# Performance work log

Measured on AMD Instinct MI355X. Metric: run time of the kernel, lower is better.

## Reference

```python
import jax, jax.numpy as jnp
import numpy as np

B, L, H, NH, NB = 16, 256, 64, 2, 2
HS = H // NH
MAXLEN, TIME_SPAN, ITEMNUM = 256, 256, 50000
NEG = -4294967295.0  # -2**32 + 1
EPS = 1e-8


def layernorm(x, g, b):
    m = jnp.mean(x, axis=-1, keepdims=True)
    v = jnp.mean((x - m) ** 2, axis=-1, keepdims=True)
    return g * (x - m) / jnp.sqrt(v + EPS) + b


def setup_inputs() -> dict:
    key = jax.random.key(0)
    ks = jax.random.split(key, 24)
    s = 0.02
    inp = {
        "seqs_data": jax.random.randint(ks[0], (B, L), 0, ITEMNUM, dtype=jnp.int32),
        "seqs": jax.random.normal(ks[1], (B, L, H), dtype=jnp.float32),
        "positions": jax.random.randint(ks[2], (B, L), 0, MAXLEN, dtype=jnp.int32),
        "time_matrices": jax.random.randint(ks[3], (B, L, L), 0, TIME_SPAN + 1, dtype=jnp.int32),
        "abs_pos_K_tab": jax.random.normal(ks[4], (MAXLEN, H)) * s,
        "abs_pos_V_tab": jax.random.normal(ks[5], (MAXLEN, H)) * s,
        "time_K_tab": jax.random.normal(ks[6], (TIME_SPAN + 1, H)) * s,
        "time_V_tab": jax.random.normal(ks[7], (TIME_SPAN + 1, H)) * s,
        "Qw": jax.random.normal(ks[8], (NB, H, H)) * s,
        "Qb": jnp.zeros((NB, H)),
        "Kw": jax.random.normal(ks[9], (NB, H, H)) * s,
        "Kb": jnp.zeros((NB, H)),
        "Vw": jax.random.normal(ks[10], (NB, H, H)) * s,
        "Vb": jnp.zeros((NB, H)),
        "ln1_g": jnp.ones((NB, H)), "ln1_b": jnp.zeros((NB, H)),
        "ln2_g": jnp.ones((NB, H)), "ln2_b": jnp.zeros((NB, H)),
        "ffn_W1": jax.random.normal(ks[11], (NB, H, H)) * s,
        "ffn_b1": jnp.zeros((NB, H)),
        "ffn_W2": jax.random.normal(ks[12], (NB, H, H)) * s,
        "ffn_b2": jnp.zeros((NB, H)),
        "last_g": jnp.ones((H,)), "last_b": jnp.zeros((H,)),
    }
    return inp


def _forward(seqs_data, seqs, positions, time_matrices,
             abs_pos_K_tab, abs_pos_V_tab, time_K_tab, time_V_tab,
             Qw, Qb, Kw, Kb, Vw, Vb, ln1_g, ln1_b, ln2_g, ln2_b,
             ffn_W1, ffn_b1, ffn_W2, ffn_b2, last_g, last_b):
    # abs-pos embeddings with padding_idx=0 (zero row, no grad flow to it)
    pos_keep = (positions != 0)[..., None].astype(seqs.dtype)
    abs_pos_K = abs_pos_K_tab[positions] * pos_keep            # [B,L,H]
    abs_pos_V = abs_pos_V_tab[positions] * pos_keep
    time_K = time_K_tab[time_matrices]                         # [B,L,L,H]
    time_V = time_V_tab[time_matrices]
    tmK = time_K.reshape(B, L, L, NH, HS)
    tmV = time_V.reshape(B, L, L, NH, HS)
    aK = abs_pos_K.reshape(B, L, NH, HS)
    aV = abs_pos_V.reshape(B, L, NH, HS)

    timeline_mask = (seqs_data == ITEMNUM - 1)                 # [B,L] True = pad
    keep = (~timeline_mask)[..., None].astype(seqs.dtype)
    seqs = seqs * keep
    causal = ~jnp.tril(jnp.ones((L, L), dtype=bool))           # [L,L] upper tri
    full_mask = timeline_mask[:, None, :, None] | causal[None, None]  # [B,1,L,L]

    for i in range(NB):
        q_in = layernorm(seqs, ln1_g[i], ln1_b[i])
        Q = (q_in @ Qw[i].T + Qb[i]).reshape(B, L, NH, HS)
        K = (seqs @ Kw[i].T + Kb[i]).reshape(B, L, NH, HS)
        V = (seqs @ Vw[i].T + Vb[i]).reshape(B, L, NH, HS)
        aw = (jnp.einsum('blhd,bmhd->bhlm', Q, K)
              + jnp.einsum('blhd,bmhd->bhlm', Q, aK)
              + jnp.einsum('blmhd,blhd->bhlm', tmK, Q)) / (HS ** 0.5)
        aw = jnp.where(full_mask, NEG, aw)
        A = jax.nn.softmax(aw, axis=-1)                        # [B,NH,L,L]
        out = (jnp.einsum('bhlm,bmhd->blhd', A, V)
               + jnp.einsum('bhlm,bmhd->blhd', A, aV)
               + jnp.einsum('bhlm,blmhd->blhd', A, tmV)).reshape(B, L, H)
        seqs = q_in + out
        seqs = layernorm(seqs, ln2_g[i], ln2_b[i])
        h = jax.nn.relu(seqs @ ffn_W1[i].T + ffn_b1[i])
        seqs = (h @ ffn_W2[i].T + ffn_b2[i]) + seqs
        seqs = seqs * keep
    return layernorm(seqs, last_g, last_b)


def reference(seqs_data, seqs, positions, time_matrices,
              abs_pos_K_tab, abs_pos_V_tab, time_K_tab, time_V_tab,
              Qw, Qb, Kw, Kb, Vw, Vb, ln1_g, ln1_b, ln2_g, ln2_b,
              ffn_W1, ffn_b1, ffn_W2, ffn_b2, last_g, last_b):
    return _forward(seqs_data, seqs, positions, time_matrices,
                    abs_pos_K_tab, abs_pos_V_tab, time_K_tab, time_V_tab,
                    Qw, Qb, Kw, Kb, Vw, Vb, ln1_g, ln1_b, ln2_g, ln2_b,
                    ffn_W1, ffn_b1, ffn_W2, ffn_b2, last_g, last_b)
```

## Files before the change

### kernel.cpp

```cpp
#include <hip/hip_runtime.h>
#include <math.h>

#define BATCH 16
#define SEQL  256
#define HDIM  64
#define NBLK  2
#define PADID 49999
#define NEGV  -4294967295.0f
#define LNEPS 1e-8f
#define INV_SQRT_HS 0.17677669529663687f
#define TKC   257
#define TKTLD 260
#define QG    4

__device__ __forceinline__ float waveReduceSum(float v) {
#pragma unroll
    for (int o = 32; o > 0; o >>= 1) v += __shfl_xor(v, o);
    return v;
}

__global__ __launch_bounds__(256) void setup_kernel(
    const float* __restrict__ Qw, const float* __restrict__ Kw,
    const float* __restrict__ Vw, const float* __restrict__ W1,
    const float* __restrict__ W2, const float* __restrict__ tKtab,
    float* __restrict__ QwT, float* __restrict__ KwT, float* __restrict__ VwT,
    float* __restrict__ W1T, float* __restrict__ W2T, float* __restrict__ tKtabT)
{
    __shared__ float tile[64][65];
    const int tid = threadIdx.x;
    const int blk = blockIdx.x;
    if (blk < 10) {
        const float* srcs[10] = {Qw, Qw+4096, Kw, Kw+4096, Vw, Vw+4096,
                                 W1, W1+4096, W2, W2+4096};
        float*       dsts[10] = {QwT, QwT+4096, KwT, KwT+4096, VwT, VwT+4096,
                                 W1T, W1T+4096, W2T, W2T+4096};
        const float* s = srcs[blk];
        float*       d = dsts[blk];
        for (int p = 0; p < 16; ++p) {
            int r = p*4 + (tid>>6), c = tid&63;
            tile[r][c] = s[r*64 + c];
        }
        __syncthreads();
        for (int p = 0; p < 16; ++p) {
            int mth = p*4 + (tid>>6), t = tid&63;
            d[mth*64 + t] = tile[t][mth];
        }
    } else {
        const int s0 = (blk - 10) * 64;
        const int nrows = min(64, TKC - s0);
        for (int p = 0; p < 16; ++p) {
            int rr = p*4 + (tid>>6), c = tid&63;
            if (rr < nrows) tile[rr][c] = tKtab[(size_t)(s0+rr)*64 + c];
        }
        __syncthreads();
        for (int p = 0; p < 16; ++p) {
            int dd = p*4 + (tid>>6), cc = tid&63;
            if (cc < nrows) tKtabT[dd*TKTLD + s0 + cc] = tile[cc][dd];
        }
    }
}

__global__ __launch_bounds__(256) void prep_kernel(
    const float* __restrict__ xin, const int* __restrict__ seqs_data,
    const int* __restrict__ positions,
    const float* __restrict__ QwT, const float* __restrict__ Qb,
    const float* __restrict__ KwT, const float* __restrict__ Kb,
    const float* __restrict__ VwT, const float* __restrict__ Vb,
    const float* __restrict__ g1, const float* __restrict__ b1,
    const float* __restrict__ apK, const float* __restrict__ apV,
    float* __restrict__ q_in, float* __restrict__ Qo,
    float* __restrict__ KpT, float* __restrict__ Vp)
{
    const int w = threadIdx.x >> 6;
    const int t = threadIdx.x & 63;
    const int row0 = blockIdx.x * 4;
    const int row = row0 + w;
    float x = xin[(size_t)row * HDIM + t];
    if (seqs_data[row] == PADID) x = 0.f;

    float mean = waveReduceSum(x) * (1.f / HDIM);
    float d = x - mean;
    float var = waveReduceSum(d * d) * (1.f / HDIM);
    float q = g1[t] * d / sqrtf(var + LNEPS) + b1[t];

    __shared__ float xs[4][HDIM];
    __shared__ float qs[4][HDIM];
    __shared__ float kx[HDIM][5];
    xs[w][t] = x; qs[w][t] = q;
    q_in[(size_t)row * HDIM + t] = q;

    int pos = positions[row];
    float aK = pos ? apK[(size_t)pos * HDIM + t] : 0.f;
    float aV = pos ? apV[(size_t)pos * HDIM + t] : 0.f;

    float aq = 0.f, ak = 0.f, av = 0.f;
#pragma unroll 16
    for (int mth = 0; mth < 64; ++mth) {
        float qm = qs[w][mth], xm = xs[w][mth];
        aq += qm * QwT[mth*64 + t];
        ak += xm * KwT[mth*64 + t];
        av += xm * VwT[mth*64 + t];
    }
    Qo[(size_t)row * HDIM + t] = aq + Qb[t];
    Vp[(size_t)row * HDIM + t] = av + Vb[t] + aV;
    kx[t][w] = ak + Kb[t] + aK;
    __syncthreads();
    const int f = threadIdx.x >> 2, j = threadIdx.x & 3;
    KpT[(size_t)f * 4096 + row0 + j] = kx[f][j];
}

__global__ __launch_bounds__(256) void attn_kernel(
    const float* __restrict__ Qo, const float* __restrict__ KpT,
    const float* __restrict__ Vp, const float* __restrict__ q_in,
    const int* __restrict__ seqs_data, const int* __restrict__ tmat,
    const float* __restrict__ tVtab, const float* __restrict__ tKtabT,
    float* __restrict__ x2)
{
    const int hw  = blockIdx.x;
    const int blk = (hw & 7) * 128 + (hw >> 3);
    const int b   = blk >> 6;
    const int l0  = (blk & 63) << 2;
    const int row0 = b * SEQL + l0;
    const int tid = threadIdx.x;
    const int m = tid;
    const int lane = tid & 63, wv = tid >> 6;

    __shared__ float qs_l[QG][HDIM];
    __shared__ float Tk_l[QG][2][TKTLD];
    __shared__ float A_s[QG][2][SEQL];
    __shared__ float Wl[QG][2][TKTLD];
    __shared__ float outred[4][QG][HDIM];
    __shared__ float redm[QG][2][4];
    __shared__ float reds[QG][2][4];

    for (int k = tid; k < QG*2*TKTLD; k += 256) ((float*)Wl)[k] = 0.f;
    qs_l[tid >> 6][tid & 63] = Qo[(size_t)(row0 + (tid >> 6)) * HDIM + (tid & 63)];
    __syncthreads();

    for (int c = tid; c < TKC; c += 256) {
        float a00 = 0.f, a10 = 0.f, a20 = 0.f, a30 = 0.f;
        float a01 = 0.f, a11 = 0.f, a21 = 0.f, a31 = 0.f;
#pragma unroll 8
        for (int dd = 0; dd < 32; ++dd) {
            float tt = tKtabT[dd*TKTLD + c];
            a00 += tt * qs_l[0][dd]; a10 += tt * qs_l[1][dd];
            a20 += tt * qs_l[2][dd]; a30 += tt * qs_l[3][dd];
        }
#pragma unroll 8
        for (int dd = 32; dd < 64; ++dd) {
            float tt = tKtabT[dd*TKTLD + c];
            a01 += tt * qs_l[0][dd]; a11 += tt * qs_l[1][dd];
            a21 += tt * qs_l[2][dd]; a31 += tt * qs_l[3][dd];
        }
        Tk_l[0][0][c] = a00; Tk_l[1][0][c] = a10; Tk_l[2][0][c] = a20; Tk_l[3][0][c] = a30;
        Tk_l[0][1][c] = a01; Tk_l[1][1][c] = a11; Tk_l[2][1][c] = a21; Tk_l[3][1][c] = a31;
    }

    bool qpad[QG]; bool anypad = false;
#pragma unroll
    for (int li = 0; li < QG; ++li) {
        qpad[li] = (seqs_data[row0 + li] == PADID);
        anypad |= qpad[li];
    }
    const int lmax = l0 + QG - 1;

    float kp[64];
    if ((m <= lmax) || anypad) {
#pragma unroll
        for (int dd = 0; dd < 64; ++dd)
            kp[dd] = KpT[(size_t)dd * 4096 + b * SEQL + m];
    } else {
#pragma unroll
        for (int dd = 0; dd < 64; ++dd) kp[dd] = 0.f;
    }
    int tmc[QG];
#pragma unroll
    for (int li = 0; li < QG; ++li)
        tmc[li] = tmat[(size_t)(row0 + li) * SEQL + m];
    __syncthreads();

    float p0v[QG], p1v[QG];
    const bool waveAllMasked = (wv * 64 > lmax) && !anypad;
#pragma unroll
    for (int li = 0; li < QG; ++li) {
        float s0, s1;
        if (waveAllMasked) {
            s0 = NEGV; s1 = NEGV;
        } else {
            const float4* q4 = (const float4*)&qs_l[li][0];
            s0 = 0.f; s1 = 0.f;
#pragma unroll
            for (int jj = 0; jj < 8; ++jj) {
                float4 qv = q4[jj];
                s0 += kp[4*jj+0]*qv.x + kp[4*jj+1]*qv.y + kp[4*jj+2]*qv.z + kp[4*jj+3]*qv.w;
            }
#pragma unroll
            for (int jj = 8; jj < 16; ++jj) {
                float4 qv = q4[jj];
                s1 += kp[4*jj+0]*qv.x + kp[4*jj+1]*qv.y + kp[4*jj+2]*qv.z + kp[4*jj+3]*qv.w;
            }
            s0 = (s0 + Tk_l[li][0][tmc[li]]) * INV_SQRT_HS;
            s1 = (s1 + Tk_l[li][1][tmc[li]]) * INV_SQRT_HS;
            const bool masked = (m > l0 + li) || qpad[li];
            s0 = masked ? NEGV : s0;
            s1 = masked ? NEGV : s1;
        }
        p0v[li] = s0; p1v[li] = s1;
    }
#pragma unroll
    for (int li = 0; li < QG; ++li) {
        float a0 = p0v[li], a1 = p1v[li];
#pragma unroll
        for (int o = 32; o > 0; o >>= 1) {
            a0 = fmaxf(a0, __shfl_xor(a0, o));
            a1 = fmaxf(a1, __shfl_xor(a1, o));
        }
        if (lane == 0) { redm[li][0][wv] = a0; redm[li][1][wv] = a1; }
    }
    __syncthreads();
#pragma unroll
    for (int li = 0; li < QG; ++li) {
        float m0 = fmaxf(fmaxf(redm[li][0][0], redm[li][0][1]),
                         fmaxf(redm[li][0][2], redm[li][0][3]));
        float m1 = fmaxf(fmaxf(redm[li][1][0], redm[li][1][1]),
                         fmaxf(redm[li][1][2], redm[li][1][3]));
        float e0 = __expf(p0v[li] - m0), e1 = __expf(p1v[li] - m1);
        p0v[li] = e0; p1v[li] = e1;
        float t0 = waveReduceSum(e0), t1 = waveReduceSum(e1);
        if (lane == 0) { reds[li][0][wv] = t0; reds[li][1][wv] = t1; }
    }
    __syncthreads();
#pragma unroll
    for (int li = 0; li < QG; ++li) {
        float sum0 = reds[li][0][0] + reds[li][0][1] + reds[li][0][2] + reds[li][0][3];
        float sum1 = reds[li][1][0] + reds[li][1][1] + reds[li][1][2] + reds[li][1][3];
        float a0 = p0v[li] / sum0;
        float a1 = p1v[li] / sum1;
        A_s[li][0][m] = a0;
        A_s[li][1][m] = a1;
        if (a0 != 0.f) atomicAdd(&Wl[li][0][tmc[li]], a0);
        if (a1 != 0.f) atomicAdd(&Wl[li][1][tmc[li]], a1);
    }
    __syncthreads();

    const int hd = lane, chunk = wv;
    const int h = hd >> 5;
    float acc0 = 0.f, acc1 = 0.f, acc2 = 0.f, acc3 = 0.f;

    const int mend = anypad ? SEQL : (lmax + 1 < SEQL ? lmax + 1 : SEQL);
    const float* vpb = Vp + (size_t)(b * SEQL) * HDIM + hd;
    int mm = chunk;
    for (; mm + 12 < mend; mm += 16) {
        float v0 = vpb[(size_t)(mm)    * HDIM];
        float v1 = vpb[(size_t)(mm+4)  * HDIM];
        float v2 = vpb[(size_t)(mm+8)  * HDIM];
        float v3 = vpb[(size_t)(mm+12) * HDIM];
        acc0 += A_s[0][h][mm]*v0 + A_s[0][h][mm+4]*v1 + A_s[0][h][mm+8]*v2 + A_s[0][h][mm+12]*v3;
        acc1 += A_s[1][h][mm]*v0 + A_s[1][h][mm+4]*v1 + A_s[1][h][mm+8]*v2 + A_s[1][h][mm+12]*v3;
        acc2 += A_s[2][h][mm]*v0 + A_s[2][h][mm+4]*v1 + A_s[2][h][mm+8]*v2 + A_s[2][h][mm+12]*v3;
        acc3 += A_s[3][h][mm]*v0 + A_s[3][h][mm+4]*v1 + A_s[3][h][mm+8]*v2 + A_s[3][h][mm+12]*v3;
    }
    for (; mm < mend; mm += 4) {
        float vp = vpb[(size_t)mm * HDIM];
        acc0 += A_s[0][h][mm]*vp; acc1 += A_s[1][h][mm]*vp;
        acc2 += A_s[2][h][mm]*vp; acc3 += A_s[3][h][mm]*vp;
    }
    const float* tvb = tVtab + hd;
    int c = chunk;
    for (; c + 12 < TKC; c += 16) {
        float t0 = tvb[(size_t)(c)    * HDIM];
        float t1 = tvb[(size_t)(c+4)  * HDIM];
        float t2 = tvb[(size_t)(c+8)  * HDIM];
        float t3 = tvb[(size_t)(c+12) * HDIM];
        acc0 += Wl[0][h][c]*t0 + Wl[0][h][c+4]*t1 + Wl[0][h][c+8]*t2 + Wl[0][h][c+12]*t3;
        acc1 += Wl[1][h][c]*t0 + Wl[1][h][c+4]*t1 + Wl[1][h][c+8]*t2 + Wl[1][h][c+12]*t3;
        acc2 += Wl[2][h][c]*t0 + Wl[2][h][c+4]*t1 + Wl[2][h][c+8]*t2 + Wl[2][h][c+12]*t3;
        acc3 += Wl[3][h][c]*t0 + Wl[3][h][c+4]*t1 + Wl[3][h][c+8]*t2 + Wl[3][h][c+12]*t3;
    }
    for (; c < TKC; c += 4) {
        float tv = tvb[(size_t)c * HDIM];
        acc0 += Wl[0][h][c]*tv; acc1 += Wl[1][h][c]*tv;
        acc2 += Wl[2][h][c]*tv; acc3 += Wl[3][h][c]*tv;
    }
    outred[chunk][0][hd] = acc0;
    outred[chunk][1][hd] = acc1;
    outred[chunk][2][hd] = acc2;
    outred[chunk][3][hd] = acc3;
    __syncthreads();
    {
        const int li = tid >> 6, dcol = tid & 63;
        const int row = row0 + li;
        float o = outred[0][li][dcol] + outred[1][li][dcol]
                + outred[2][li][dcol] + outred[3][li][dcol];
        x2[(size_t)row * HDIM + dcol] = q_in[(size_t)row * HDIM + dcol] + o;
    }
}

__global__ __launch_bounds__(256) void ffnprep_kernel(
    const float* __restrict__ x2, const int* __restrict__ seqs_data,
    const int* __restrict__ positions,
    const float* __restrict__ g2, const float* __restrict__ bg2,
    const float* __restrict__ W1T, const float* __restrict__ bb1,
    const float* __restrict__ W2T, const float* __restrict__ bb2,
    const float* __restrict__ g1n, const float* __restrict__ b1n,
    const float* __restrict__ QwT, const float* __restrict__ Qb,
    const float* __restrict__ KwT, const float* __restrict__ Kb,
    const float* __restrict__ VwT, const float* __restrict__ Vb,
    const float* __restrict__ apK, const float* __restrict__ apV,
    float* __restrict__ q_in, float* __restrict__ Qo,
    float* __restrict__ KpT, float* __restrict__ Vp)
{
    const int w = threadIdx.x >> 6;
    const int t = threadIdx.x & 63;
    const int row0 = blockIdx.x * 4;
    const int row = row0 + w;
    float x = x2[(size_t)row * HDIM + t];
    float mean = waveReduceSum(x) * (1.f / HDIM);
    float d = x - mean;
    float var = waveReduceSum(d * d) * (1.f / HDIM);
    float s = g2[t] * d / sqrtf(var + LNEPS) + bg2[t];

    __shared__ float ss[4][HDIM];
    __shared__ float hs[4][HDIM];
    __shared__ float kx[HDIM][5];
    ss[w][t] = s;
    float acc = 0.f;
#pragma unroll 16
    for (int mth = 0; mth < 64; ++mth)
        acc += ss[w][mth] * W1T[mth*64 + t];
    float hval = fmaxf(acc + bb1[t], 0.f);
    hs[w][t] = hval;
    float acc2 = 0.f;
#pragma unroll 16
    for (int mth = 0; mth < 64; ++mth)
        acc2 += hs[w][mth] * W2T[mth*64 + t];
    float y = acc2 + bb2[t] + s;
    if (seqs_data[row] == PADID) y = 0.f;

    float mean2 = waveReduceSum(y) * (1.f / HDIM);
    float d2 = y - mean2;
    float var2 = waveReduceSum(d2 * d2) * (1.f / HDIM);
    float q = g1n[t] * d2 / sqrtf(var2 + LNEPS) + b1n[t];

    ss[w][t] = y;
    hs[w][t] = q;
    q_in[(size_t)row * HDIM + t] = q;

    int pos = positions[row];
    float aK = pos ? apK[(size_t)pos * HDIM + t] : 0.f;
    float aV = pos ? apV[(size_t)pos * HDIM + t] : 0.f;

    float aq = 0.f, ak = 0.f, av = 0.f;
#pragma unroll 16
    for (int mth = 0; mth < 64; ++mth) {
        float qm = hs[w][mth], ym = ss[w][mth];
        aq += qm * QwT[mth*64 + t];
        ak += ym * KwT[mth*64 + t];
        av += ym * VwT[mth*64 + t];
    }
    Qo[(size_t)row * HDIM + t] = aq + Qb[t];
    Vp[(size_t)row * HDIM + t] = av + Vb[t] + aV;
    kx[t][w] = ak + Kb[t] + aK;
    __syncthreads();
    const int f = threadIdx.x >> 2, j = threadIdx.x & 3;
    KpT[(size_t)f * 4096 + row0 + j] = kx[f][j];
}

__global__ __launch_bounds__(256) void ffnfinal_kernel(
    const float* __restrict__ x2, const int* __restrict__ seqs_data,
    const float* __restrict__ g2, const float* __restrict__ bg2,
    const float* __restrict__ W1T, const float* __restrict__ bb1,
    const float* __restrict__ W2T, const float* __restrict__ bb2,
    const float* __restrict__ lg, const float* __restrict__ lb,
    float* __restrict__ dout)
{
    const int w = threadIdx.x >> 6;
    const int t = threadIdx.x & 63;
    const int row = blockIdx.x * 4 + w;
    float x = x2[(size_t)row * HDIM + t];
    float mean = waveReduceSum(x) * (1.f / HDIM);
    float d = x - mean;
    float var = waveReduceSum(d * d) * (1.f / HDIM);
    float s = g2[t] * d / sqrtf(var + LNEPS) + bg2[t];

    __shared__ float ss[4][HDIM];
    __shared__ float hs[4][HDIM];
    ss[w][t] = s;
    float acc = 0.f;
#pragma unroll 16
    for (int mth = 0; mth < 64; ++mth)
        acc += ss[w][mth] * W1T[mth*64 + t];
    float hval = fmaxf(acc + bb1[t], 0.f);
    hs[w][t] = hval;
    float acc2 = 0.f;
#pragma unroll 16
    for (int mth = 0; mth < 64; ++mth)
        acc2 += hs[w][mth] * W2T[mth*64 + t];
    float y = acc2 + bb2[t] + s;
    if (seqs_data[row] == PADID) y = 0.f;
    float m2 = waveReduceSum(y) * (1.f / HDIM);
    float dd = y - m2;
    float v2 = waveReduceSum(dd * dd) * (1.f / HDIM);
    dout[(size_t)row * HDIM + t] = lg[t] * dd / sqrtf(v2 + LNEPS) + lb[t];
}

extern "C" void kernel_launch(void* const* d_in, const int* in_sizes, int n_in,
                              void* d_out, int out_size, void* d_ws, size_t ws_size,
                              hipStream_t stream) {
    const int*   seqs_data = (const int*)d_in[0];
    const float* seqs      = (const float*)d_in[1];
    const int*   positions = (const int*)d_in[2];
    const int*   tmat      = (const int*)d_in[3];
    const float* apK       = (const float*)d_in[4];
    const float* apV       = (const float*)d_in[5];
    const float* tKtab     = (const float*)d_in[6];
    const float* tVtab     = (const float*)d_in[7];
    const float* Qw = (const float*)d_in[8];
    const float* Qb = (const float*)d_in[9];
    const float* Kw = (const float*)d_in[10];
    const float* Kb = (const float*)d_in[11];
    const float* Vw = (const float*)d_in[12];
    const float* Vb = (const float*)d_in[13];
    const float* g1 = (const float*)d_in[14];
    const float* b1 = (const float*)d_in[15];
    const float* g2 = (const float*)d_in[16];
    const float* b2 = (const float*)d_in[17];
    const float* W1 = (const float*)d_in[18];
    const float* fb1 = (const float*)d_in[19];
    const float* W2 = (const float*)d_in[20];
    const float* fb2 = (const float*)d_in[21];
    const float* lastg = (const float*)d_in[22];
    const float* lastb = (const float*)d_in[23];

    const size_t N = (size_t)BATCH * SEQL * HDIM;
    float* ws    = (float*)d_ws;
    float* x     = ws;
    float* q_in  = ws + 1 * N;
    float* Qo    = ws + 2 * N;
    float* Vp    = ws + 3 * N;
    float* KpT   = ws + 4 * N;
    float* wtbase = ws + 5 * N;
    float* QwT = wtbase;
    float* KwT = wtbase + 8192;
    float* VwT = wtbase + 16384;
    float* W1T = wtbase + 24576;
    float* W2T = wtbase + 32768;
    float* tKtabT = wtbase + 40960;

    const int rows = BATCH * SEQL;

    setup_kernel<<<15, 256, 0, stream>>>(Qw, Kw, Vw, W1, W2, tKtab,
                                         QwT, KwT, VwT, W1T, W2T, tKtabT);

    prep_kernel<<<rows / 4, 256, 0, stream>>>(
        seqs, seqs_data, positions,
        QwT, Qb, KwT, Kb, VwT, Vb, g1, b1,
        apK, apV, q_in, Qo, KpT, Vp);

    attn_kernel<<<rows / QG, 256, 0, stream>>>(
        Qo, KpT, Vp, q_in, seqs_data, tmat, tVtab, tKtabT, x);

    ffnprep_kernel<<<rows / 4, 256, 0, stream>>>(
        x, seqs_data, positions,
        g2, b2, W1T, fb1, W2T, fb2,
        g1 + HDIM, b1 + HDIM,
        QwT + 4096, Qb + HDIM, KwT + 4096, Kb + HDIM, VwT + 4096, Vb + HDIM,
        apK, apV, q_in, Qo, KpT, Vp);

    attn_kernel<<<rows / QG, 256, 0, stream>>>(
        Qo, KpT, Vp, q_in, seqs_data, tmat, tVtab, tKtabT, x);

    ffnfinal_kernel<<<rows / 4, 256, 0, stream>>>(
        x, seqs_data,
        g2 + HDIM, b2 + HDIM, W1T + 4096, fb1 + HDIM, W2T + 4096, fb2 + HDIM,
        lastg, lastb, (float*)d_out);
}
```

Before: 206.8 us.

## Split attention work across heads with 512-thread blocks

The attention kernel now launches 512 threads per block, with each half handling one head's scores (32 dims) for all key positions. This replaces the per-thread 64-register kp array with a streamed 32-element dot product. The AV and time-value accumulation is spread over 8 chunks instead of 4, and the tmat/pad loads move ahead of the time-key precompute. The aim is to cut register pressure and raise parallelism, at the cost of more threads sharing the same shared-memory reductions and an extra sync.

```diff
diff --git a/kernel.cpp b/kernel.cpp
--- a/kernel.cpp
+++ b/kernel.cpp
@@ -109,7 +109,7 @@
     KpT[(size_t)f * 4096 + row0 + j] = kx[f][j];
 }
 
-__global__ __launch_bounds__(256) void attn_kernel(
+__global__ __launch_bounds__(512) void attn_kernel(
     const float* __restrict__ Qo, const float* __restrict__ KpT,
     const float* __restrict__ Vp, const float* __restrict__ q_in,
     const int* __restrict__ seqs_data, const int* __restrict__ tmat,
@@ -122,24 +122,40 @@
     const int l0  = (blk & 63) << 2;
     const int row0 = b * SEQL + l0;
     const int tid = threadIdx.x;
-    const int m = tid;
-    const int lane = tid & 63, wv = tid >> 6;
+    const int m   = tid & 255;
+    const int h   = tid >> 8;
+    const int lane = tid & 63;
+    const int wv  = tid >> 6;
+    const int mw  = wv & 3;
 
     __shared__ float qs_l[QG][HDIM];
     __shared__ float Tk_l[QG][2][TKTLD];
     __shared__ float A_s[QG][2][SEQL];
     __shared__ float Wl[QG][2][TKTLD];
-    __shared__ float outred[4][QG][HDIM];
+    __shared__ float outred[8][QG][HDIM];
     __shared__ float redm[QG][2][4];
     __shared__ float reds[QG][2][4];
 
-    for (int k = tid; k < QG*2*TKTLD; k += 256) ((float*)Wl)[k] = 0.f;
-    qs_l[tid >> 6][tid & 63] = Qo[(size_t)(row0 + (tid >> 6)) * HDIM + (tid & 63)];
-    __syncthreads();
-
-    for (int c = tid; c < TKC; c += 256) {
-        float a00 = 0.f, a10 = 0.f, a20 = 0.f, a30 = 0.f;
-        float a01 = 0.f, a11 = 0.f, a21 = 0.f, a31 = 0.f;
+    for (int k = tid; k < QG*2*TKTLD; k += 512) ((float*)Wl)[k] = 0.f;
+    if (tid < QG*HDIM)
+        qs_l[tid >> 6][tid & 63] = Qo[(size_t)(row0 + (tid >> 6)) * HDIM + (tid & 63)];
+
+    bool qpad[QG]; bool anypad = false;
+#pragma unroll
+    for (int li = 0; li < QG; ++li) {
+        qpad[li] = (seqs_data[row0 + li] == PADID);
+        anypad |= qpad[li];
+    }
+    const int lmax = l0 + QG - 1;
+    int tmc[QG];
+#pragma unroll
+    for (int li = 0; li < QG; ++li)
+        tmc[li] = tmat[(size_t)(row0 + li) * SEQL + m];
+    __syncthreads();
+
+    if (tid < TKC) {
+        const int c = tid;
+        float a00=0.f,a10=0.f,a20=0.f,a30=0.f, a01=0.f,a11=0.f,a21=0.f,a31=0.f;
 #pragma unroll 8
         for (int dd = 0; dd < 32; ++dd) {
             float tt = tKtabT[dd*TKTLD + c];
@@ -152,146 +168,111 @@
             a01 += tt * qs_l[0][dd]; a11 += tt * qs_l[1][dd];
             a21 += tt * qs_l[2][dd]; a31 += tt * qs_l[3][dd];
         }
-        Tk_l[0][0][c] = a00; Tk_l[1][0][c] = a10; Tk_l[2][0][c] = a20; Tk_l[3][0][c] = a30;
-        Tk_l[0][1][c] = a01; Tk_l[1][1][c] = a11; Tk_l[2][1][c] = a21; Tk_l[3][1][c] = a31;
-    }
-
-    bool qpad[QG]; bool anypad = false;
+        Tk_l[0][0][c]=a00; Tk_l[1][0][c]=a10; Tk_l[2][0][c]=a20; Tk_l[3][0][c]=a30;
+        Tk_l[0][1][c]=a01; Tk_l[1][1][c]=a11; Tk_l[2][1][c]=a21; Tk_l[3][1][c]=a31;
+    }
+    __syncthreads();
+
+    float sv[QG];
+    const bool waveAllMasked = (mw * 64 > lmax) && !anypad;
+    if (waveAllMasked) {
+#pragma unroll
+        for (int li = 0; li < QG; ++li) sv[li] = NEGV;
+    } else {
+        float s0=0.f, s1=0.f, s2=0.f, s3=0.f;
+        const float* kpb = KpT + (size_t)(h*32) * 4096 + (size_t)b * SEQL + m;
+        const float* q0 = &qs_l[0][h*32];
+        const float* q1 = &qs_l[1][h*32];
+        const float* q2 = &qs_l[2][h*32];
+        const float* q3 = &qs_l[3][h*32];
+#pragma unroll 8
+        for (int dd = 0; dd < 32; ++dd) {
+            float kv = kpb[(size_t)dd * 4096];
+            s0 += kv * q0[dd]; s1 += kv * q1[dd];
+            s2 += kv * q2[dd]; s3 += kv * q3[dd];
+        }
+        float sarr[QG] = {s0, s1, s2, s3};
+#pragma unroll
+        for (int li = 0; li < QG; ++li) {
+            float s = (sarr[li] + Tk_l[li][h][tmc[li]]) * INV_SQRT_HS;
+            const bool masked = (m > l0 + li) || qpad[li];
+            sv[li] = masked ? NEGV : s;
+        }
+    }
 #pragma unroll
     for (int li = 0; li < QG; ++li) {
-        qpad[li] = (seqs_data[row0 + li] == PADID);
-        anypad |= qpad[li];
-    }
-    const int lmax = l0 + QG - 1;
-
-    float kp[64];
-    if ((m <= lmax) || anypad) {
-#pragma unroll
-        for (int dd = 0; dd < 64; ++dd)
-            kp[dd] = KpT[(size_t)dd * 4096 + b * SEQL + m];
-    } else {
-#pragma unroll
-        for (int dd = 0; dd < 64; ++dd) kp[dd] = 0.f;
-    }
-    int tmc[QG];
-#pragma unroll
-    for (int li = 0; li < QG; ++li)
-        tmc[li] = tmat[(size_t)(row0 + li) * SEQL + m];
-    __syncthreads();
-
-    float p0v[QG], p1v[QG];
-    const bool waveAllMasked = (wv * 64 > lmax) && !anypad;
+        float a = sv[li];
+#pragma unroll
+        for (int o = 32; o > 0; o >>= 1) a = fmaxf(a, __shfl_xor(a, o));
+        if (lane == 0) redm[li][h][mw] = a;
+    }
+    __syncthreads();
 #pragma unroll
     for (int li = 0; li < QG; ++li) {
-        float s0, s1;
-        if (waveAllMasked) {
-            s0 = NEGV; s1 = NEGV;
-        } else {
-            const float4* q4 = (const float4*)&qs_l[li][0];
-            s0 = 0.f; s1 = 0.f;
-#pragma unroll
-            for (int jj = 0; jj < 8; ++jj) {
-                float4 qv = q4[jj];
-                s0 += kp[4*jj+0]*qv.x + kp[4*jj+1]*qv.y + kp[4*jj+2]*qv.z + kp[4*jj+3]*qv.w;
-            }
-#pragma unroll
-            for (int jj = 8; jj < 16; ++jj) {
-                float4 qv = q4[jj];
-                s1 += kp[4*jj+0]*qv.x + kp[4*jj+1]*qv.y + kp[4*jj+2]*qv.z + kp[4*jj+3]*qv.w;
-            }
-            s0 = (s0 + Tk_l[li][0][tmc[li]]) * INV_SQRT_HS;
-            s1 = (s1 + Tk_l[li][1][tmc[li]]) * INV_SQRT_HS;
-            const bool masked = (m > l0 + li) || qpad[li];
-            s0 = masked ? NEGV : s0;
-            s1 = masked ? NEGV : s1;
-        }
-        p0v[li] = s0; p1v[li] = s1;
-    }
+        float mx = fmaxf(fmaxf(redm[li][h][0], redm[li][h][1]),
+                         fmaxf(redm[li][h][2], redm[li][h][3]));
+        float e = __expf(sv[li] - mx);
+        sv[li] = e;
+        float t = waveReduceSum(e);
+        if (lane == 0) reds[li][h][mw] = t;
+    }
+    __syncthreads();
 #pragma unroll
     for (int li = 0; li < QG; ++li) {
-        float a0 = p0v[li], a1 = p1v[li];
-#pragma unroll
-        for (int o = 32; o > 0; o >>= 1) {
-            a0 = fmaxf(a0, __shfl_xor(a0, o));
-            a1 = fmaxf(a1, __shfl_xor(a1, o));
-        }
-        if (lane == 0) { redm[li][0][wv] = a0; redm[li][1][wv] = a1; }
-    }
-    __syncthreads();
-#pragma unroll
-    for (int li = 0; li < QG; ++li) {
-        float m0 = fmaxf(fmaxf(redm[li][0][0], redm[li][0][1]),
-                         fmaxf(redm[li][0][2], redm[li][0][3]));
-        float m1 = fmaxf(fmaxf(redm[li][1][0], redm[li][1][1]),
-                         fmaxf(redm[li][1][2], redm[li][1][3]));
-        float e0 = __expf(p0v[li] - m0), e1 = __expf(p1v[li] - m1);
-        p0v[li] = e0; p1v[li] = e1;
-        float t0 = waveReduceSum(e0), t1 = waveReduceSum(e1);
-        if (lane == 0) { reds[li][0][wv] = t0; reds[li][1][wv] = t1; }
-    }
-    __syncthreads();
-#pragma unroll
-    for (int li = 0; li < QG; ++li) {
-        float sum0 = reds[li][0][0] + reds[li][0][1] + reds[li][0][2] + reds[li][0][3];
-        float sum1 = reds[li][1][0] + reds[li][1][1] + reds[li][1][2] + reds[li][1][3];
-        float a0 = p0v[li] / sum0;
-        float a1 = p1v[li] / sum1;
-        A_s[li][0][m] = a0;
-        A_s[li][1][m] = a1;
-        if (a0 != 0.f) atomicAdd(&Wl[li][0][tmc[li]], a0);
-        if (a1 != 0.f) atomicAdd(&Wl[li][1][tmc[li]], a1);
-    }
-    __syncthreads();
-
-    const int hd = lane, chunk = wv;
-    const int h = hd >> 5;
+        float sum = reds[li][h][0] + reds[li][h][1] + reds[li][h][2] + reds[li][h][3];
+        float a = sv[li] / sum;
+        A_s[li][h][m] = a;
+        if (a != 0.f) atomicAdd(&Wl[li][h][tmc[li]], a);
+    }
+    __syncthreads();
+
+    const int hd = tid & 63, chunk = tid >> 6;
+    const int hh = hd >> 5;
     float acc0 = 0.f, acc1 = 0.f, acc2 = 0.f, acc3 = 0.f;
 
     const int mend = anypad ? SEQL : (lmax + 1 < SEQL ? lmax + 1 : SEQL);
     const float* vpb = Vp + (size_t)(b * SEQL) * HDIM + hd;
     int mm = chunk;
-    for (; mm + 12 < mend; mm += 16) {
-        float v0 = vpb[(size_t)(mm)    * HDIM];
-        float v1 = vpb[(size_t)(mm+4)  * HDIM];
-        float v2 = vpb[(size_t)(mm+8)  * HDIM];
-        float v3 = vpb[(size_t)(mm+12) * HDIM];
-        acc0 += A_s[0][h][mm]*v0 + A_s[0][h][mm+4]*v1 + A_s[0][h][mm+8]*v2 + A_s[0][h][mm+12]*v3;
-        acc1 += A_s[1][h][mm]*v0 + A_s[1][h][mm+4]*v1 + A_s[1][h][mm+8]*v2 + A_s[1][h][mm+12]*v3;
-        acc2 += A_s[2][h][mm]*v0 + A_s[2][h][mm+4]*v1 + A_s[2][h][mm+8]*v2 + A_s[2][h][mm+12]*v3;
-        acc3 += A_s[3][h][mm]*v0 + A_s[3][h][mm+4]*v1 + A_s[3][h][mm+8]*v2 + A_s[3][h][mm+12]*v3;
-    }
-    for (; mm < mend; mm += 4) {
+    for (; mm + 8 < mend; mm += 16) {
+        float v0 = vpb[(size_t)(mm)   * HDIM];
+        float v1 = vpb[(size_t)(mm+8) * HDIM];
+        acc0 += A_s[0][hh][mm]*v0 + A_s[0][hh][mm+8]*v1;
+        acc1 += A_s[1][hh][mm]*v0 + A_s[1][hh][mm+8]*v1;
+        acc2 += A_s[2][hh][mm]*v0 + A_s[2][hh][mm+8]*v1;
+        acc3 += A_s[3][hh][mm]*v0 + A_s[3][hh][mm+8]*v1;
+    }
+    for (; mm < mend; mm += 8) {
         float vp = vpb[(size_t)mm * HDIM];
-        acc0 += A_s[0][h][mm]*vp; acc1 += A_s[1][h][mm]*vp;
-        acc2 += A_s[2][h][mm]*vp; acc3 += A_s[3][h][mm]*vp;
+        acc0 += A_s[0][hh][mm]*vp; acc1 += A_s[1][hh][mm]*vp;
+        acc2 += A_s[2][hh][mm]*vp; acc3 += A_s[3][hh][mm]*vp;
     }
     const float* tvb = tVtab + hd;
     int c = chunk;
-    for (; c + 12 < TKC; c += 16) {
-        float t0 = tvb[(size_t)(c)    * HDIM];
-        float t1 = tvb[(size_t)(c+4)  * HDIM];
-        float t2 = tvb[(size_t)(c+8)  * HDIM];
-        float t3 = tvb[(size_t)(c+12) * HDIM];
-        acc0 += Wl[0][h][c]*t0 + Wl[0][h][c+4]*t1 + Wl[0][h][c+8]*t2 + Wl[0][h][c+12]*t3;
-        acc1 += Wl[1][h][c]*t0 + Wl[1][h][c+4]*t1 + Wl[1][h][c+8]*t2 + Wl[1][h][c+12]*t3;
-        acc2 += Wl[2][h][c]*t0 + Wl[2][h][c+4]*t1 + Wl[2][h][c+8]*t2 + Wl[2][h][c+12]*t3;
-        acc3 += Wl[3][h][c]*t0 + Wl[3][h][c+4]*t1 + Wl[3][h][c+8]*t2 + Wl[3][h][c+12]*t3;
-    }
-    for (; c < TKC; c += 4) {
+    for (; c + 8 < TKC; c += 16) {
+        float t0 = tvb[(size_t)(c)   * HDIM];
+        float t1 = tvb[(size_t)(c+8) * HDIM];
+        acc0 += Wl[0][hh][c]*t0 + Wl[0][hh][c+8]*t1;
+        acc1 += Wl[1][hh][c]*t0 + Wl[1][hh][c+8]*t1;
+        acc2 += Wl[2][hh][c]*t0 + Wl[2][hh][c+8]*t1;
+        acc3 += Wl[3][hh][c]*t0 + Wl[3][hh][c+8]*t1;
+    }
+    for (; c < TKC; c += 8) {
         float tv = tvb[(size_t)c * HDIM];
-        acc0 += Wl[0][h][c]*tv; acc1 += Wl[1][h][c]*tv;
-        acc2 += Wl[2][h][c]*tv; acc3 += Wl[3][h][c]*tv;
+        acc0 += Wl[0][hh][c]*tv; acc1 += Wl[1][hh][c]*tv;
+        acc2 += Wl[2][hh][c]*tv; acc3 += Wl[3][hh][c]*tv;
     }
     outred[chunk][0][hd] = acc0;
     outred[chunk][1][hd] = acc1;
     outred[chunk][2][hd] = acc2;
     outred[chunk][3][hd] = acc3;
     __syncthreads();
-    {
+    if (tid < 256) {
         const int li = tid >> 6, dcol = tid & 63;
         const int row = row0 + li;
         float o = outred[0][li][dcol] + outred[1][li][dcol]
-                + outred[2][li][dcol] + outred[3][li][dcol];
+                + outred[2][li][dcol] + outred[3][li][dcol]
+                + outred[4][li][dcol] + outred[5][li][dcol]
+                + outred[6][li][dcol] + outred[7][li][dcol];
         x2[(size_t)row * HDIM + dcol] = q_in[(size_t)row * HDIM + dcol] + o;
     }
 }
@@ -457,7 +438,7 @@
         QwT, Qb, KwT, Kb, VwT, Vb, g1, b1,
         apK, apV, q_in, Qo, KpT, Vp);
 
-    attn_kernel<<<rows / QG, 256, 0, stream>>>(
+    attn_kernel<<<rows / QG, 512, 0, stream>>>(
         Qo, KpT, Vp, q_in, seqs_data, tmat, tVtab, tKtabT, x);
 
     ffnprep_kernel<<<rows / 4, 256, 0, stream>>>(
@@ -467,7 +448,7 @@
         QwT + 4096, Qb + HDIM, KwT + 4096, Kb + HDIM, VwT + 4096, Vb + HDIM,
         apK, apV, q_in, Qo, KpT, Vp);
 
-    attn_kernel<<<rows / QG, 256, 0, stream>>>(
+    attn_kernel<<<rows / QG, 512, 0, stream>>>(
         Qo, KpT, Vp, q_in, seqs_data, tmat, tVtab, tKtabT, x);
 
     ffnfinal_kernel<<<rows / 4, 256, 0, stream>>>(
```

After: 205.9 us. Within noise of the previous version (-0.4%).
